# Performance work log

Measured on AMD Instinct MI355X. Metric: run time of the kernel, lower is better.

## Reference

```python
import jax, jax.numpy as jnp
import numpy as np

M, D, S, K, DIN = 512, 10, 16384, 1024, 784  # test points, classes, jacobian dim, n_eigh, input dim


def setup_inputs() -> dict:
    key = jax.random.key(0)
    k0, k1, k2, k3, k4 = jax.random.split(key, 5)
    X_test = jax.random.normal(k0, (M, DIN), dtype=jnp.float32)
    Jz = jax.random.normal(k1, (M, D, S), dtype=jnp.float32) * 0.02      # backend.jacobians(X_test)
    v = jax.random.normal(k2, (S, K), dtype=jnp.float32) * 0.02          # self.v from fit()
    A = jax.random.normal(k3, (K, K), dtype=jnp.float32) * 0.02
    G_inv = 0.5 * (A + A.T) + jnp.eye(K, dtype=jnp.float32)              # symmetric, like an inverse PSD matrix
    W_net = jax.random.normal(k4, (DIN, D), dtype=jnp.float32) * 0.02    # stand-in for self.net
    return {"X_test": X_test, "Jz": Jz, "v": v, "G_inv": G_inv, "W_net": W_net}


def reference(X_test, Jz, v, G_inv, W_net):
    # phi: (d, m, k) -- per-class ELLA features of each test point
    phi = jnp.einsum('mds,sk->dmk', Jz, v)
    # Full (class, class, n, m) covariance tensor, exactly as the torch module computes it
    K_test = jnp.einsum('ank,kg,bmg->abnm', phi, G_inv, phi)
    mean = X_test @ W_net                                # self.net(X_test)
    var = jnp.diagonal(K_test, axis1=-2, axis2=-1)       # (d, d, n) -- discards off-diagonal n,m
    return mean, jnp.transpose(var, (2, 0, 1))           # (n, d, d)
```

## Files before the change

kernel.cpp:

```cpp
#include <hip/hip_runtime.h>
#include <hip/hip_bf16.h>

#define M_PTS 512
#define D_CLS 10
#define S_DIM 16384
#define K_DIM 1024
#define DIN_  784
#define PHI_ELEMS (5120 * 1024)

typedef short  bf16x8  __attribute__((ext_vector_type(8)));
typedef float  f32x4   __attribute__((ext_vector_type(4)));
typedef ushort ushort8 __attribute__((ext_vector_type(8)));

__device__ __forceinline__ ushort f2bfu(float f) {
    __bf16 h = (__bf16)f;
    return __builtin_bit_cast(ushort, h);
}
__device__ __forceinline__ float bfu2f(ushort u) {
    uint x = (uint)u << 16;
    return __builtin_bit_cast(float, x);
}

__global__ __launch_bounds__(64) void mean_kernel(const float* __restrict__ X,
                                                  const float* __restrict__ W,
                                                  float* __restrict__ out) {
    int m = blockIdx.x;
    int lane = threadIdx.x;
    float acc[D_CLS];
#pragma unroll
    for (int d = 0; d < D_CLS; ++d) acc[d] = 0.f;
    for (int i = lane; i < DIN_; i += 64) {
        float x = X[(size_t)m * DIN_ + i];
#pragma unroll
        for (int d = 0; d < D_CLS; ++d) acc[d] += x * W[i * D_CLS + d];
    }
#pragma unroll
    for (int d = 0; d < D_CLS; ++d) {
        float v = acc[d];
        for (int off = 32; off > 0; off >>= 1) v += __shfl_down(v, off);
        if (lane == 0) out[(size_t)m * D_CLS + d] = v;
    }
}

__global__ __launch_bounds__(256) void cvt_a(const float* __restrict__ src,
                                             ushort* __restrict__ dst, int n8) {
    for (int i = blockIdx.x * 256 + threadIdx.x; i < n8; i += gridDim.x * 256) {
        float4 a = reinterpret_cast<const float4*>(src)[2 * i];
        float4 b = reinterpret_cast<const float4*>(src)[2 * i + 1];
        ushort8 o;
        o[0] = f2bfu(a.x); o[1] = f2bfu(a.y); o[2] = f2bfu(a.z); o[3] = f2bfu(a.w);
        o[4] = f2bfu(b.x); o[5] = f2bfu(b.y); o[6] = f2bfu(b.z); o[7] = f2bfu(b.w);
        reinterpret_cast<ushort8*>(dst)[i] = o;
    }
}

__global__ __launch_bounds__(256) void cvt_bt(const float* __restrict__ v,
                                              ushort* __restrict__ bt) {
    __shared__ float tile[64][65];
    const int kt = blockIdx.x;
    const int ct = blockIdx.y;
    const int t  = threadIdx.x;
    const int col4 = t & 15, row = t >> 4;
#pragma unroll
    for (int i = 0; i < 4; ++i) {
        int r = row + 16 * i;
        float4 v4 = *reinterpret_cast<const float4*>(
            v + (size_t)(kt * 64 + r) * K_DIM + ct * 64 + col4 * 4);
        tile[r][col4 * 4 + 0] = v4.x; tile[r][col4 * 4 + 1] = v4.y;
        tile[r][col4 * 4 + 2] = v4.z; tile[r][col4 * 4 + 3] = v4.w;
    }
    __syncthreads();
#pragma unroll
    for (int i = 0; i < 2; ++i) {
        int cid = i * 256 + t;
        int c = cid >> 3, kc = cid & 7;
        ushort8 o;
#pragma unroll
        for (int j = 0; j < 8; ++j) o[j] = f2bfu(tile[kc * 8 + j][c]);
        *reinterpret_cast<ushort8*>(bt + (size_t)(ct * 64 + c) * S_DIM +
                                    kt * 64 + kc * 8) = o;
    }
}

template <int SD, int KSP>
__global__ __launch_bounds__(256, 3) void gemm_bs(const ushort* __restrict__ A,
                                                  const ushort* __restrict__ BT,
                                                  ushort* __restrict__ Cout) {
    __shared__ ushort As[3][4096];
    __shared__ ushort Bs[3][4096];

    const int nwg = 320 * KSP;
    const int lid = blockIdx.x;
    const int swz = (lid & 7) * (nwg >> 3) + (lid >> 3);
    const int kp  = swz / 320;
    const int rem = swz - kp * 320;
    const int bm  = rem >> 3;
    const int bn  = rem & 7;
    const int KSTEPS = SD / 32 / KSP;
    const int kbase  = kp * (SD / KSP);

    const int t  = threadIdx.x;
    const int l  = t & 63;
    const int wm = (t >> 7) & 1;
    const int wn = (t >> 6) & 1;
    const int lr = l & 15;
    const int kq = l >> 4;

    const ushort* Ablk = A  + (size_t)(bm * 128) * SD + kbase;
    const ushort* Bblk = BT + (size_t)(bn * 128) * SD + kbase;

    f32x4 acc[4][4];
#pragma unroll
    for (int i = 0; i < 4; ++i)
#pragma unroll
        for (int j = 0; j < 4; ++j) acc[i][j] = (f32x4)0.f;

#define GSTAGE(BUF, S, SRC, DST)                                                \
    { _Pragma("unroll") for (int i = 0; i < 2; ++i) {                           \
        const int cch = i * 256 + t;                                            \
        const int r = cch >> 2, sl = cch & 3;                                   \
        const ushort* gp = SRC + (size_t)r * SD + (S) * 32 +                    \
                           ((sl ^ ((r >> 1) & 3)) << 3);                        \
        ushort* lp = &DST[BUF][(i * 256 + (t & 192)) * 8];                      \
        __builtin_amdgcn_global_load_lds(                                       \
            (const __attribute__((address_space(1))) void*)gp,                  \
            (__attribute__((address_space(3))) void*)lp, 16, 0, 0);             \
      } }

#define GCOMPUTE(BUF)                                                           \
    { bf16x8 fa[4], fb[4];                                                      \
      _Pragma("unroll") for (int mi = 0; mi < 4; ++mi) {                        \
        const int r = wm * 64 + mi * 16 + lr;                                   \
        fa[mi] = *reinterpret_cast<const bf16x8*>(                              \
            &As[BUF][(r * 4 + (kq ^ ((r >> 1) & 3))) * 8]);                     \
      }                                                                         \
      _Pragma("unroll") for (int ni = 0; ni < 4; ++ni) {                        \
        const int c = wn * 64 + ni * 16 + lr;                                   \
        fb[ni] = *reinterpret_cast<const bf16x8*>(                              \
            &Bs[BUF][(c * 4 + (kq ^ ((c >> 1) & 3))) * 8]);                     \
      }                                                                         \
      _Pragma("unroll") for (int ni = 0; ni < 4; ++ni)                          \
        _Pragma("unroll") for (int mi = 0; mi < 4; ++mi)                        \
          acc[mi][ni] = __builtin_amdgcn_mfma_f32_16x16x32_bf16(                \
              fa[mi], fb[ni], acc[mi][ni], 0, 0, 0);                            \
    }

    GSTAGE(0, 0, Ablk, As)
    GSTAGE(0, 0, Bblk, Bs)
    GSTAGE(1, 1, Ablk, As)
    GSTAGE(1, 1, Bblk, Bs)
    asm volatile("s_waitcnt vmcnt(4)" ::: "memory");
    __builtin_amdgcn_s_barrier();
    __builtin_amdgcn_sched_barrier(0);

    for (int s = 0; s < KSTEPS - 2; ++s) {
        const int sb = (s + 2) % 3, cb = s % 3;
        GSTAGE(sb, s + 2, Ablk, As)
        GSTAGE(sb, s + 2, Bblk, Bs)
        __builtin_amdgcn_s_setprio(1);
        GCOMPUTE(cb)
        __builtin_amdgcn_s_setprio(0);
        __builtin_amdgcn_sched_barrier(0);
        asm volatile("s_waitcnt vmcnt(4)" ::: "memory");
        __builtin_amdgcn_s_barrier();
        __builtin_amdgcn_sched_barrier(0);
    }
    {
        __builtin_amdgcn_s_setprio(1);
        GCOMPUTE((KSTEPS - 2) % 3)
        __builtin_amdgcn_s_setprio(0);
        __builtin_amdgcn_sched_barrier(0);
        asm volatile("s_waitcnt vmcnt(0)" ::: "memory");
        __builtin_amdgcn_s_barrier();
        __builtin_amdgcn_sched_barrier(0);
        GCOMPUTE((KSTEPS - 1) % 3)
    }

    ushort* C = Cout + (size_t)kp * PHI_ELEMS;
#pragma unroll
    for (int mi = 0; mi < 4; ++mi) {
        int orow = bm * 128 + wm * 64 + mi * 16 + kq * 4;
#pragma unroll
        for (int ni = 0; ni < 4; ++ni) {
            int ocol = bn * 128 + wn * 64 + ni * 16 + lr;
            ushort* cp = C + (size_t)orow * K_DIM + ocol;
#pragma unroll
            for (int rr = 0; rr < 4; ++rr)
                cp[(size_t)rr * K_DIM] = f2bfu(acc[mi][ni][rr]);
        }
    }
#undef GSTAGE
#undef GCOMPUTE
}

template <int SD, int KSP>
__global__ __launch_bounds__(256, 3) void gemm_bb(const ushort* __restrict__ A,
                                                  const ushort* __restrict__ BT,
                                                  float* __restrict__ Cout) {
    __shared__ ushort As[3][4096];
    __shared__ ushort Bs[3][4096];

    const int nwg = 320 * KSP;
    const int lid = blockIdx.x;
    const int swz = (lid & 7) * (nwg >> 3) + (lid >> 3);
    const int kp  = swz / 320;
    const int rem = swz - kp * 320;
    const int bm  = rem >> 3;
    const int bn  = rem & 7;
    const int KSTEPS = SD / 32 / KSP;
    const int kbase  = kp * (SD / KSP);

    const int t  = threadIdx.x;
    const int l  = t & 63;
    const int wm = (t >> 7) & 1;
    const int wn = (t >> 6) & 1;
    const int lr = l & 15;
    const int kq = l >> 4;

    const ushort* Ablk = A  + (size_t)(bm * 128) * SD + kbase;
    const ushort* Bblk = BT + (size_t)(bn * 128) * SD + kbase;

    f32x4 acc[4][4];
#pragma unroll
    for (int i = 0; i < 4; ++i)
#pragma unroll
        for (int j = 0; j < 4; ++j) acc[i][j] = (f32x4)0.f;

#define GSTAGE(BUF, S, SRC, DST)                                                \
    { _Pragma("unroll") for (int i = 0; i < 2; ++i) {                           \
        const int cch = i * 256 + t;                                            \
        const int r = cch >> 2, sl = cch & 3;                                   \
        const ushort* gp = SRC + (size_t)r * SD + (S) * 32 +                    \
                           ((sl ^ ((r >> 1) & 3)) << 3);                        \
        ushort* lp = &DST[BUF][(i * 256 + (t & 192)) * 8];                      \
        __builtin_amdgcn_global_load_lds(                                       \
            (const __attribute__((address_space(1))) void*)gp,                  \
            (__attribute__((address_space(3))) void*)lp, 16, 0, 0);             \
      } }

#define GCOMPUTE(BUF)                                                           \
    { bf16x8 fa[4], fb[4];                                                      \
      _Pragma("unroll") for (int mi = 0; mi < 4; ++mi) {                        \
        const int r = wm * 64 + mi * 16 + lr;                                   \
        fa[mi] = *reinterpret_cast<const bf16x8*>(                              \
            &As[BUF][(r * 4 + (kq ^ ((r >> 1) & 3))) * 8]);                     \
      }                                                                         \
      _Pragma("unroll") for (int ni = 0; ni < 4; ++ni) {                        \
        const int c = wn * 64 + ni * 16 + lr;                                   \
        fb[ni] = *reinterpret_cast<const bf16x8*>(                              \
            &Bs[BUF][(c * 4 + (kq ^ ((c >> 1) & 3))) * 8]);                     \
      }                                                                         \
      _Pragma("unroll") for (int ni = 0; ni < 4; ++ni)                          \
        _Pragma("unroll") for (int mi = 0; mi < 4; ++mi)                        \
          acc[mi][ni] = __builtin_amdgcn_mfma_f32_16x16x32_bf16(                \
              fa[mi], fb[ni], acc[mi][ni], 0, 0, 0);                            \
    }

    GSTAGE(0, 0, Ablk, As)
    GSTAGE(0, 0, Bblk, Bs)
    GSTAGE(1, 1, Ablk, As)
    GSTAGE(1, 1, Bblk, Bs)
    asm volatile("s_waitcnt vmcnt(4)" ::: "memory");
    __builtin_amdgcn_s_barrier();
    __builtin_amdgcn_sched_barrier(0);

    for (int s = 0; s < KSTEPS - 2; ++s) {
        const int sb = (s + 2) % 3, cb = s % 3;
        GSTAGE(sb, s + 2, Ablk, As)
        GSTAGE(sb, s + 2, Bblk, Bs)
        __builtin_amdgcn_s_setprio(1);
        GCOMPUTE(cb)
        __builtin_amdgcn_s_setprio(0);
        __builtin_amdgcn_sched_barrier(0);
        asm volatile("s_waitcnt vmcnt(4)" ::: "memory");
        __builtin_amdgcn_s_barrier();
        __builtin_amdgcn_sched_barrier(0);
    }
    {
        __builtin_amdgcn_s_setprio(1);
        GCOMPUTE((KSTEPS - 2) % 3)
        __builtin_amdgcn_s_setprio(0);
        __builtin_amdgcn_sched_barrier(0);
        asm volatile("s_waitcnt vmcnt(0)" ::: "memory");
        __builtin_amdgcn_s_barrier();
        __builtin_amdgcn_sched_barrier(0);
        GCOMPUTE((KSTEPS - 1) % 3)
    }

    float* C = Cout + (size_t)kp * PHI_ELEMS;
#pragma unroll
    for (int mi = 0; mi < 4; ++mi) {
        int orow = bm * 128 + wm * 64 + mi * 16 + kq * 4;
#pragma unroll
        for (int ni = 0; ni < 4; ++ni) {
            int ocol = bn * 128 + wn * 64 + ni * 16 + lr;
            float* cp = C + (size_t)orow * K_DIM + ocol;
#pragma unroll
            for (int rr = 0; rr < 4; ++rr) cp[(size_t)rr * K_DIM] = acc[mi][ni][rr];
        }
    }
#undef GSTAGE
#undef GCOMPUTE
}

template <int KSP>
__global__ __launch_bounds__(256) void phi_reduceN(const ushort* __restrict__ slabs,
                                                   ushort* __restrict__ phib) {
    const int n8 = PHI_ELEMS / 8;
    for (int i = blockIdx.x * 256 + threadIdx.x; i < n8; i += gridDim.x * 256) {
        float s[8] = {0.f, 0.f, 0.f, 0.f, 0.f, 0.f, 0.f, 0.f};
#pragma unroll
        for (int p = 0; p < KSP; ++p) {
            ushort8 u = reinterpret_cast<const ushort8*>(
                slabs + (size_t)p * PHI_ELEMS)[i];
#pragma unroll
            for (int j = 0; j < 8; ++j) s[j] += bfu2f(u[j]);
        }
        ushort8 o;
#pragma unroll
        for (int j = 0; j < 8; ++j) o[j] = f2bfu(s[j]);
        reinterpret_cast<ushort8*>(phib)[i] = o;
    }
}

__global__ __launch_bounds__(256) void var_contract_b(const float* __restrict__ T,
                                                      const ushort* __restrict__ P,
                                                      float* __restrict__ out) {
    __shared__ float red[4][56];
    const int n = blockIdx.x, t = threadIdx.x, lane = t & 63, wid = t >> 6;
    const float*  Tn = T + (size_t)n * D_CLS * K_DIM;
    const ushort* Pn = P + (size_t)n * D_CLS * K_DIM;
    float Ta[D_CLS][4], Pb[D_CLS][4];
#pragma unroll
    for (int a = 0; a < D_CLS; ++a)
#pragma unroll
        for (int j = 0; j < 4; ++j) {
            Ta[a][j] = Tn[a * K_DIM + t + 256 * j];
            Pb[a][j] = bfu2f(Pn[a * K_DIM + t + 256 * j]);
        }
    int p = 0;
#pragma unroll
    for (int a = 0; a < D_CLS; ++a)
#pragma unroll
        for (int b = 0; b <= a; ++b, ++p) {
            float s = Ta[a][0] * Pb[b][0] + Ta[a][1] * Pb[b][1]
                    + Ta[a][2] * Pb[b][2] + Ta[a][3] * Pb[b][3];
#pragma unroll
            for (int off = 32; off > 0; off >>= 1) s += __shfl_down(s, off);
            if (lane == 0) red[wid][p] = s;
        }
    __syncthreads();
    if (t < 55) {
        int a = 0;
        while ((a + 1) * (a + 2) / 2 <= t) ++a;
        int b = t - a * (a + 1) / 2;
        float s = red[0][t] + red[1][t] + red[2][t] + red[3][t];
        float* vout = out + M_PTS * D_CLS + (size_t)n * D_CLS * D_CLS;
        vout[a * D_CLS + b] = s;
        vout[b * D_CLS + a] = s;
    }
}

extern "C" void kernel_launch(void* const* d_in, const int* in_sizes, int n_in,
                              void* d_out, int out_size, void* d_ws, size_t ws_size,
                              hipStream_t stream) {
    const float* X  = (const float*)d_in[0];
    const float* Jz = (const float*)d_in[1];
    const float* v  = (const float*)d_in[2];
    const float* G  = (const float*)d_in[3];
    const float* W  = (const float*)d_in[4];
    float* out = (float*)d_out;
    float* ws  = (float*)d_ws;

    const size_t PHB  = (size_t)PHI_ELEMS * 2;
    const size_t A_B  = (size_t)5120 * S_DIM * 2;
    const size_t BT_B = (size_t)K_DIM * S_DIM * 2;
    const size_t G_B  = (size_t)K_DIM * K_DIM * 2;
    const size_t NEED4 = 4 * PHB + BT_B + G_B + A_B;
    const size_t NEED1 = 1 * PHB + BT_B + G_B + A_B;
    (void)NEED1;

    hipLaunchKernelGGL(mean_kernel, dim3(M_PTS), dim3(64), 0, stream, X, W, out);

    const int KSP = (ws_size >= NEED4) ? 4 : 1;
    ushort* slabs = (ushort*)ws;
    ushort* vTb   = slabs + (size_t)KSP * PHI_ELEMS;
    ushort* Gb    = vTb + (size_t)K_DIM * S_DIM;
    ushort* Abf   = Gb + (size_t)K_DIM * K_DIM;
    ushort* phib  = slabs;
    float*  T     = (KSP == 4) ? (float*)(slabs + (size_t)2 * PHI_ELEMS)
                               : (float*)Abf;

    hipLaunchKernelGGL(cvt_a, dim3(2048), dim3(256), 0, stream,
                       Jz, Abf, 5120 * S_DIM / 8);
    hipLaunchKernelGGL(cvt_bt, dim3(256, 16), dim3(256), 0, stream, v, vTb);
    hipLaunchKernelGGL(cvt_a, dim3(256), dim3(256), 0, stream,
                       G, Gb, K_DIM * K_DIM / 8);
    if (KSP == 4) {
        hipLaunchKernelGGL((gemm_bs<S_DIM, 4>), dim3(1280), dim3(256), 0,
                           stream, Abf, vTb, slabs);
        hipLaunchKernelGGL(phi_reduceN<4>, dim3(1024), dim3(256), 0, stream,
                           slabs, phib);
    } else {
        hipLaunchKernelGGL((gemm_bs<S_DIM, 1>), dim3(320), dim3(256), 0,
                           stream, Abf, vTb, slabs);
    }
    hipLaunchKernelGGL((gemm_bb<K_DIM, 1>), dim3(320), dim3(256), 0, stream,
                       phib, Gb, T);
    hipLaunchKernelGGL(var_contract_b, dim3(M_PTS), dim3(256), 0, stream,
                       T, phib, out);
}
```

Baseline: 409.1 us.

## Fuse fp32-to-bf16 conversion of Jz into the phi GEMM A-operand load

Drops the separate cvt_a pass that turned the large Jz tensor into bf16 in workspace. The new gemm_cv kernel reads fp32 Jz tiles into registers, converts them to bf16 and writes them into swizzled LDS. B still arrives through direct global-to-LDS loads, now with double buffering instead of a triple-buffered asynchronous pipeline. This avoids writing and re-reading a 160MB bf16 copy, at the cost of doubling A-operand read bandwidth inside the GEMM and adding register-staged conversion work that may be less overlapped.

After: 424.0 us. +3.7%, slower.

```diff
diff --git a/kernel.cpp b/kernel.cpp
--- a/kernel.cpp
+++ b/kernel.cpp
@@ -82,10 +82,141 @@
     }
 }
 
-template <int SD, int KSP>
-__global__ __launch_bounds__(256, 3) void gemm_bs(const ushort* __restrict__ A,
+template <int KSP>
+__global__ __launch_bounds__(256, 4) void gemm_cv(const float* __restrict__ A,
                                                   const ushort* __restrict__ BT,
                                                   ushort* __restrict__ Cout) {
+    __shared__ ushort As[2][4096];
+    __shared__ ushort Bs[2][4096];
+
+    const int nwg = 320 * KSP;
+    const int lid = blockIdx.x;
+    const int swz = (lid & 7) * (nwg >> 3) + (lid >> 3);
+    const int kp  = swz / 320;
+    const int rem = swz - kp * 320;
+    const int bm  = rem >> 3;
+    const int bn  = rem & 7;
+    const int KSTEPS = 512 / KSP;
+    const int kbase  = kp * (S_DIM / KSP);
+
+    const int t  = threadIdx.x;
+    const int l  = t & 63;
+    const int wm = (t >> 7) & 1;
+    const int wn = (t >> 6) & 1;
+    const int lr = l & 15;
+    const int kq = l >> 4;
+
+    const float*  Ablk = A  + (size_t)(bm * 128) * S_DIM + kbase;
+    const ushort* Bblk = BT + (size_t)(bn * 128) * S_DIM + kbase;
+
+    const int   ar   = t >> 2;
+    const int   csrc = (t & 3) ^ ((t >> 3) & 3);
+    const float* ag0 = Ablk + (size_t)ar * S_DIM + csrc * 8;
+    const float* ag1 = ag0 + (size_t)64 * S_DIM;
+
+    float4 rA[4], rB[4];
+
+    f32x4 acc[4][4];
+#pragma unroll
+    for (int i = 0; i < 4; ++i)
+#pragma unroll
+        for (int j = 0; j < 4; ++j) acc[i][j] = (f32x4)0.f;
+
+#define LOADA(P, S)                                                             \
+    { P[0] = *reinterpret_cast<const float4*>(ag0 + (size_t)(S) * 32);          \
+      P[1] = *reinterpret_cast<const float4*>(ag0 + (size_t)(S) * 32 + 4);      \
+      P[2] = *reinterpret_cast<const float4*>(ag1 + (size_t)(S) * 32);          \
+      P[3] = *reinterpret_cast<const float4*>(ag1 + (size_t)(S) * 32 + 4); }
+
+#define WRITEA(BUF, P)                                                          \
+    { ushort8 o0, o1;                                                           \
+      o0[0] = f2bfu(P[0].x); o0[1] = f2bfu(P[0].y);                             \
+      o0[2] = f2bfu(P[0].z); o0[3] = f2bfu(P[0].w);                             \
+      o0[4] = f2bfu(P[1].x); o0[5] = f2bfu(P[1].y);                             \
+      o0[6] = f2bfu(P[1].z); o0[7] = f2bfu(P[1].w);                             \
+      o1[0] = f2bfu(P[2].x); o1[1] = f2bfu(P[2].y);                             \
+      o1[2] = f2bfu(P[2].z); o1[3] = f2bfu(P[2].w);                             \
+      o1[4] = f2bfu(P[3].x); o1[5] = f2bfu(P[3].y);                             \
+      o1[6] = f2bfu(P[3].z); o1[7] = f2bfu(P[3].w);                             \
+      *reinterpret_cast<ushort8*>(&As[BUF][t * 8])        = o0;                 \
+      *reinterpret_cast<ushort8*>(&As[BUF][t * 8 + 2048]) = o1; }
+
+#define STAGE_B(BUF, S)                                                         \
+    { _Pragma("unroll") for (int i = 0; i < 2; ++i) {                           \
+        const int cch = i * 256 + t;                                            \
+        const int r = cch >> 2, sl = cch & 3;                                   \
+        const ushort* gp = Bblk + (size_t)r * S_DIM + (S) * 32 +                \
+                           ((sl ^ ((r >> 1) & 3)) << 3);                        \
+        ushort* lp = &Bs[BUF][(i * 256 + (t & 192)) * 8];                       \
+        __builtin_amdgcn_global_load_lds(                                       \
+            (const __attribute__((address_space(1))) void*)gp,                  \
+            (__attribute__((address_space(3))) void*)lp, 16, 0, 0);             \
+      } }
+
+#define COMPUTE(BUF)                                                            \
+    { bf16x8 fa[4], fb[4];                                                      \
+      _Pragma("unroll") for (int mi = 0; mi < 4; ++mi) {                        \
+        const int r = wm * 64 + mi * 16 + lr;                                   \
+        fa[mi] = *reinterpret_cast<const bf16x8*>(                              \
+            &As[BUF][(r * 4 + (kq ^ ((r >> 1) & 3))) * 8]);                     \
+      }                                                                         \
+      _Pragma("unroll") for (int ni = 0; ni < 4; ++ni) {                        \
+        const int c = wn * 64 + ni * 16 + lr;                                   \
+        fb[ni] = *reinterpret_cast<const bf16x8*>(                              \
+            &Bs[BUF][(c * 4 + (kq ^ ((c >> 1) & 3))) * 8]);                     \
+      }                                                                         \
+      _Pragma("unroll") for (int ni = 0; ni < 4; ++ni)                          \
+        _Pragma("unroll") for (int mi = 0; mi < 4; ++mi)                        \
+          acc[mi][ni] = __builtin_amdgcn_mfma_f32_16x16x32_bf16(                \
+              fa[mi], fb[ni], acc[mi][ni], 0, 0, 0);                            \
+    }
+
+    LOADA(rA, 0)
+    STAGE_B(0, 0)
+    WRITEA(0, rA)
+    LOADA(rB, 1)
+    __syncthreads();
+
+    const int NIT2 = KSTEPS / 2;
+    for (int s2 = 0; s2 < NIT2; ++s2) {
+        const int s = 2 * s2;
+        if (s + 2 < KSTEPS) { LOADA(rA, s + 2) }
+        STAGE_B(1, s + 1)
+        WRITEA(1, rB)
+        COMPUTE(0)
+        __syncthreads();
+        if (s + 3 < KSTEPS) { LOADA(rB, s + 3) }
+        if (s + 2 < KSTEPS) {
+            STAGE_B(0, s + 2)
+            WRITEA(0, rA)
+        }
+        COMPUTE(1)
+        __syncthreads();
+    }
+
+    ushort* C = Cout + (size_t)kp * PHI_ELEMS;
+#pragma unroll
+    for (int mi = 0; mi < 4; ++mi) {
+        int orow = bm * 128 + wm * 64 + mi * 16 + kq * 4;
+#pragma unroll
+        for (int ni = 0; ni < 4; ++ni) {
+            int ocol = bn * 128 + wn * 64 + ni * 16 + lr;
+            ushort* cp = C + (size_t)orow * K_DIM + ocol;
+#pragma unroll
+            for (int rr = 0; rr < 4; ++rr)
+                cp[(size_t)rr * K_DIM] = f2bfu(acc[mi][ni][rr]);
+        }
+    }
+#undef LOADA
+#undef WRITEA
+#undef STAGE_B
+#undef COMPUTE
+}
+
+template <int SD, int KSP>
+__global__ __launch_bounds__(256, 3) void gemm_bb(const ushort* __restrict__ A,
+                                                  const ushort* __restrict__ BT,
+                                                  float* __restrict__ Cout) {
     __shared__ ushort As[3][4096];
     __shared__ ushort Bs[3][4096];
 
@@ -176,117 +307,6 @@
         GCOMPUTE((KSTEPS - 1) % 3)
     }
 
-    ushort* C = Cout + (size_t)kp * PHI_ELEMS;
-#pragma unroll
-    for (int mi = 0; mi < 4; ++mi) {
-        int orow = bm * 128 + wm * 64 + mi * 16 + kq * 4;
-#pragma unroll
-        for (int ni = 0; ni < 4; ++ni) {
-            int ocol = bn * 128 + wn * 64 + ni * 16 + lr;
-            ushort* cp = C + (size_t)orow * K_DIM + ocol;
-#pragma unroll
-            for (int rr = 0; rr < 4; ++rr)
-                cp[(size_t)rr * K_DIM] = f2bfu(acc[mi][ni][rr]);
-        }
-    }
-#undef GSTAGE
-#undef GCOMPUTE
-}
-
-template <int SD, int KSP>
-__global__ __launch_bounds__(256, 3) void gemm_bb(const ushort* __restrict__ A,
-                                                  const ushort* __restrict__ BT,
-                                                  float* __restrict__ Cout) {
-    __shared__ ushort As[3][4096];
-    __shared__ ushort Bs[3][4096];
-
-    const int nwg = 320 * KSP;
-    const int lid = blockIdx.x;
-    const int swz = (lid & 7) * (nwg >> 3) + (lid >> 3);
-    const int kp  = swz / 320;
-    const int rem = swz - kp * 320;
-    const int bm  = rem >> 3;
-    const int bn  = rem & 7;
-    const int KSTEPS = SD / 32 / KSP;
-    const int kbase  = kp * (SD / KSP);
-
-    const int t  = threadIdx.x;
-    const int l  = t & 63;
-    const int wm = (t >> 7) & 1;
-    const int wn = (t >> 6) & 1;
-    const int lr = l & 15;
-    const int kq = l >> 4;
-
-    const ushort* Ablk = A  + (size_t)(bm * 128) * SD + kbase;
-    const ushort* Bblk = BT + (size_t)(bn * 128) * SD + kbase;
-
-    f32x4 acc[4][4];
-#pragma unroll
-    for (int i = 0; i < 4; ++i)
-#pragma unroll
-        for (int j = 0; j < 4; ++j) acc[i][j] = (f32x4)0.f;
-
-#define GSTAGE(BUF, S, SRC, DST)                                                \
-    { _Pragma("unroll") for (int i = 0; i < 2; ++i) {                           \
-        const int cch = i * 256 + t;                                            \
-        const int r = cch >> 2, sl = cch & 3;                                   \
-        const ushort* gp = SRC + (size_t)r * SD + (S) * 32 +                    \
-                           ((sl ^ ((r >> 1) & 3)) << 3);                        \
-        ushort* lp = &DST[BUF][(i * 256 + (t & 192)) * 8];                      \
-        __builtin_amdgcn_global_load_lds(                                       \
-            (const __attribute__((address_space(1))) void*)gp,                  \
-            (__attribute__((address_space(3))) void*)lp, 16, 0, 0);             \
-      } }
-
-#define GCOMPUTE(BUF)                                                           \
-    { bf16x8 fa[4], fb[4];                                                      \
-      _Pragma("unroll") for (int mi = 0; mi < 4; ++mi) {                        \
-        const int r = wm * 64 + mi * 16 + lr;                                   \
-        fa[mi] = *reinterpret_cast<const bf16x8*>(                              \
-            &As[BUF][(r * 4 + (kq ^ ((r >> 1) & 3))) * 8]);                     \
-      }                                                                         \
-      _Pragma("unroll") for (int ni = 0; ni < 4; ++ni) {                        \
-        const int c = wn * 64 + ni * 16 + lr;                                   \
-        fb[ni] = *reinterpret_cast<const bf16x8*>(                              \
-            &Bs[BUF][(c * 4 + (kq ^ ((c >> 1) & 3))) * 8]);                     \
-      }                                                                         \
-      _Pragma("unroll") for (int ni = 0; ni < 4; ++ni)                          \
-        _Pragma("unroll") for (int mi = 0; mi < 4; ++mi)                        \
-          acc[mi][ni] = __builtin_amdgcn_mfma_f32_16x16x32_bf16(                \
-              fa[mi], fb[ni], acc[mi][ni], 0, 0, 0);                            \
-    }
-
-    GSTAGE(0, 0, Ablk, As)
-    GSTAGE(0, 0, Bblk, Bs)
-    GSTAGE(1, 1, Ablk, As)
-    GSTAGE(1, 1, Bblk, Bs)
-    asm volatile("s_waitcnt vmcnt(4)" ::: "memory");
-    __builtin_amdgcn_s_barrier();
-    __builtin_amdgcn_sched_barrier(0);
-
-    for (int s = 0; s < KSTEPS - 2; ++s) {
-        const int sb = (s + 2) % 3, cb = s % 3;
-        GSTAGE(sb, s + 2, Ablk, As)
-        GSTAGE(sb, s + 2, Bblk, Bs)
-        __builtin_amdgcn_s_setprio(1);
-        GCOMPUTE(cb)
-        __builtin_amdgcn_s_setprio(0);
-        __builtin_amdgcn_sched_barrier(0);
-        asm volatile("s_waitcnt vmcnt(4)" ::: "memory");
-        __builtin_amdgcn_s_barrier();
-        __builtin_amdgcn_sched_barrier(0);
-    }
-    {
-        __builtin_amdgcn_s_setprio(1);
-        GCOMPUTE((KSTEPS - 2) % 3)
-        __builtin_amdgcn_s_setprio(0);
-        __builtin_amdgcn_sched_barrier(0);
-        asm volatile("s_waitcnt vmcnt(0)" ::: "memory");
-        __builtin_amdgcn_s_barrier();
-        __builtin_amdgcn_sched_barrier(0);
-        GCOMPUTE((KSTEPS - 1) % 3)
-    }
-
     float* C = Cout + (size_t)kp * PHI_ELEMS;
 #pragma unroll
     for (int mi = 0; mi < 4; ++mi) {
@@ -373,11 +393,10 @@
     float* ws  = (float*)d_ws;
 
     const size_t PHB  = (size_t)PHI_ELEMS * 2;
-    const size_t A_B  = (size_t)5120 * S_DIM * 2;
     const size_t BT_B = (size_t)K_DIM * S_DIM * 2;
     const size_t G_B  = (size_t)K_DIM * K_DIM * 2;
-    const size_t NEED4 = 4 * PHB + BT_B + G_B + A_B;
-    const size_t NEED1 = 1 * PHB + BT_B + G_B + A_B;
+    const size_t NEED4 = 4 * PHB + BT_B + G_B;
+    const size_t NEED1 = PHB + BT_B + G_B + (size_t)PHI_ELEMS * 4;
     (void)NEED1;
 
     hipLaunchKernelGGL(mean_kernel, dim3(M_PTS), dim3(64), 0, stream, X, W, out);
@@ -386,24 +405,21 @@
     ushort* slabs = (ushort*)ws;
     ushort* vTb   = slabs + (size_t)KSP * PHI_ELEMS;
     ushort* Gb    = vTb + (size_t)K_DIM * S_DIM;
-    ushort* Abf   = Gb + (size_t)K_DIM * K_DIM;
     ushort* phib  = slabs;
     float*  T     = (KSP == 4) ? (float*)(slabs + (size_t)2 * PHI_ELEMS)
-                               : (float*)Abf;
-
-    hipLaunchKernelGGL(cvt_a, dim3(2048), dim3(256), 0, stream,
-                       Jz, Abf, 5120 * S_DIM / 8);
+                               : (float*)(Gb + (size_t)K_DIM * K_DIM);
+
     hipLaunchKernelGGL(cvt_bt, dim3(256, 16), dim3(256), 0, stream, v, vTb);
     hipLaunchKernelGGL(cvt_a, dim3(256), dim3(256), 0, stream,
                        G, Gb, K_DIM * K_DIM / 8);
     if (KSP == 4) {
-        hipLaunchKernelGGL((gemm_bs<S_DIM, 4>), dim3(1280), dim3(256), 0,
-                           stream, Abf, vTb, slabs);
+        hipLaunchKernelGGL(gemm_cv<4>, dim3(1280), dim3(256), 0, stream,
+                           Jz, vTb, slabs);
         hipLaunchKernelGGL(phi_reduceN<4>, dim3(1024), dim3(256), 0, stream,
                            slabs, phib);
     } else {
-        hipLaunchKernelGGL((gemm_bs<S_DIM, 1>), dim3(320), dim3(256), 0,
-                           stream, Abf, vTb, slabs);
+        hipLaunchKernelGGL(gemm_cv<1>, dim3(320), dim3(256), 0, stream,
+                           Jz, vTb, slabs);
     }
     hipLaunchKernelGGL((gemm_bb<K_DIM, 1>), dim3(320), dim3(256), 0, stream,
                        phib, Gb, T);
```
